# Optimization experiments

Measured on AMD Instinct MI355X. Metric: run time of the kernel, lower is better.

The kernel has to match this reference:

```python
import jax, jax.numpy as jnp
import numpy as np

N_NODES = 100000
N_EDGES = 1600000
F_IN = 128
HID = 128


def setup_inputs() -> dict:
    key = jax.random.key(0)
    ks = jax.random.split(key, 16)
    x = jax.random.normal(ks[0], (N_NODES, F_IN), dtype=jnp.float32)
    edge_index = jax.random.randint(ks[1], (2, N_EDGES), 0, N_NODES, dtype=jnp.int32)
    edge_weight = jax.random.uniform(ks[2], (N_EDGES,), dtype=jnp.float32)
    def glorot(k, fan_in, fan_out):
        s = jnp.sqrt(6.0 / (fan_in + fan_out))
        return jax.random.uniform(k, (fan_in, fan_out), dtype=jnp.float32, minval=-s, maxval=s)
    inp = {"x": x, "edge_index": edge_index, "edge_weight": edge_weight}
    dims = [(F_IN, HID), (HID, HID), (HID, HID), (HID, HID)]
    for i, (di, do) in enumerate(dims):
        inp[f"Wc{i}"] = glorot(ks[3 + i], di, do)
        inp[f"bc{i}"] = jnp.zeros((do,), dtype=jnp.float32)
    inp["Wout"] = glorot(ks[8], HID, F_IN)
    inp["bout"] = jnp.zeros((F_IN,), dtype=jnp.float32)
    return inp


def _gcn_conv(x, W, b, row, col, ew, deg_isqrt, n):
    # PyG GCNConv: h = x @ W; out = sum_{(r,c)} norm_rc * h[r] scattered to c, plus
    # self-loop term (weight 1), plus bias. norm_rc = d^-1/2[r] * ew * d^-1/2[c].
    h = x @ W
    norm = deg_isqrt[row] * ew * deg_isqrt[col]          # [E]
    agg = jax.ops.segment_sum(h[row] * norm[:, None], col, num_segments=n)
    agg = agg + h * (deg_isqrt * deg_isqrt)[:, None]      # self loops, weight 1
    return agg + b


def reference(x, edge_index, edge_weight, Wc0, bc0, Wc1, bc1, Wc2, bc2, Wc3, bc3, Wout, bout):
    n = x.shape[0]
    row, col = edge_index[0], edge_index[1]
    # degree includes self-loop weight 1 (gcn_norm with add_self_loops=True)
    deg = jax.ops.segment_sum(edge_weight, col, num_segments=n) + 1.0
    deg_isqrt = jnp.where(deg > 0, jax.lax.rsqrt(deg), 0.0)
    Ws = [Wc0, Wc1, Wc2, Wc3]
    bs = [bc0, bc1, bc2, bc3]
    h = x
    for i in range(3):
        h = jax.nn.relu(_gcn_conv(h, Ws[i], bs[i], row, col, edge_weight, deg_isqrt, n))
    h = _gcn_conv(h, Ws[3], bs[3], row, col, edge_weight, deg_isqrt, n)
    return h @ Wout + bout
```

## Files before the change

### kernel.cpp

```cpp
#include <hip/hip_runtime.h>


#define SCAN_CHUNK 1024
#define NBUCK_MAX  512
#define BCAP       6144

typedef __attribute__((ext_vector_type(8))) short bf16x8;
typedef __attribute__((ext_vector_type(4))) float f32x4;

__device__ inline unsigned bf16pack(float a, float b) {
    unsigned ua = __float_as_uint(a);
    unsigned ub = __float_as_uint(b);
    ua = (ua + 0x7fffu + ((ua >> 16) & 1u)) >> 16;
    ub = (ub + 0x7fffu + ((ub >> 16) & 1u)) & 0xffff0000u;
    return ua | ub;
}

__device__ inline void split2(float x, ushort& hi, ushort& lo) {
    unsigned u = __float_as_uint(x);
    unsigned r = (u + 0x7fffu + ((u >> 16) & 1u)) & 0xffff0000u;
    hi = (ushort)(r >> 16);
    float rem = x - __uint_as_float(r);
    unsigned u2 = __float_as_uint(rem);
    lo = (ushort)((u2 + 0x7fffu + ((u2 >> 16) & 1u)) >> 16);
}

__device__ inline void bf16x8_expand(uint4 w, float4& a, float4& b) {
    a.x = __uint_as_float(w.x << 16);
    a.y = __uint_as_float(w.x & 0xffff0000u);
    a.z = __uint_as_float(w.y << 16);
    a.w = __uint_as_float(w.y & 0xffff0000u);
    b.x = __uint_as_float(w.z << 16);
    b.y = __uint_as_float(w.z & 0xffff0000u);
    b.z = __uint_as_float(w.w << 16);
    b.w = __uint_as_float(w.w & 0xffff0000u);
}

__global__ __launch_bounds__(256) void k_prepw(const float* W0, const float* W1,
                                               const float* W2, const float* W3,
                                               const float* W4,
                                               ushort* __restrict__ hiO,
                                               ushort* __restrict__ loO) {
    const float* W = (blockIdx.x == 0) ? W0 : (blockIdx.x == 1) ? W1 :
                     (blockIdx.x == 2) ? W2 : (blockIdx.x == 3) ? W3 : W4;
    ushort* h = hiO + (size_t)blockIdx.x * 16384;
    ushort* l = loO + (size_t)blockIdx.x * 16384;
    for (int idx = threadIdx.x; idx < 4096; idx += 256) {
        int n  = idx >> 5;
        int kq = (idx & 31) * 4;
        ushort hs[4], ls[4];
#pragma unroll
        for (int j = 0; j < 4; j++) split2(W[(kq + j) * 128 + n], hs[j], ls[j]);
        *(uint2*)&h[n * 128 + kq] =
            make_uint2(hs[0] | ((unsigned)hs[1] << 16), hs[2] | ((unsigned)hs[3] << 16));
        *(uint2*)&l[n * 128 + kq] =
            make_uint2(ls[0] | ((unsigned)ls[1] << 16), ls[2] | ((unsigned)ls[3] << 16));
    }
}

__global__ __launch_bounds__(256) void k_hist(const int* __restrict__ col,
                                              int* __restrict__ hist,
                                              int E, int K, int B1, int chunk) {
    __shared__ int cnt[NBUCK_MAX];
    int b = blockIdx.x, t = threadIdx.x;
    for (int k = t; k < K; k += 256) cnt[k] = 0;
    __syncthreads();
    int e0 = b * chunk, e1 = min(e0 + chunk, E);
    for (int e = e0 + t; e < e1; e += 256) atomicAdd(&cnt[col[e] >> 8], 1);
    __syncthreads();
    for (int k = t; k < K; k += 256) hist[k * B1 + b] = cnt[k];
}

__global__ __launch_bounds__(256) void k_scan_part(const int* __restrict__ count,
                                                   int* __restrict__ partials, int n) {
    __shared__ int red[256];
    int t = threadIdx.x;
    int base = blockIdx.x * SCAN_CHUNK + t * 4;
    int s = 0;
#pragma unroll
    for (int j = 0; j < 4; j++) {
        int i = base + j;
        if (i < n) s += count[i];
    }
    red[t] = s;
    __syncthreads();
    for (int off = 128; off > 0; off >>= 1) {
        if (t < off) red[t] += red[t + off];
        __syncthreads();
    }
    if (t == 0) partials[blockIdx.x] = red[0];
}

__global__ __launch_bounds__(1024) void k_scan_top(const int* __restrict__ partials,
                                                   int* __restrict__ blockOff,
                                                   int* __restrict__ result,
                                                   int nb, int n) {
    __shared__ int sums[1024];
    int t = threadIdx.x;
    int v = (t < nb) ? partials[t] : 0;
    sums[t] = v;
    __syncthreads();
    for (int off = 1; off < 1024; off <<= 1) {
        int u = (t >= off) ? sums[t - off] : 0;
        __syncthreads();
        sums[t] += u;
        __syncthreads();
    }
    if (t < nb) blockOff[t] = sums[t] - v;
    if (t == nb - 1) result[n] = sums[t];
}

__global__ __launch_bounds__(256) void k_scan_out(const int* __restrict__ count,
                                                  const int* __restrict__ blockOff,
                                                  int* __restrict__ result, int n) {
    __shared__ int sums[256];
    int t = threadIdx.x;
    int base = blockIdx.x * SCAN_CHUNK + t * 4;
    int c[4]; int s = 0;
#pragma unroll
    for (int j = 0; j < 4; j++) {
        int i = base + j;
        c[j] = (i < n) ? count[i] : 0;
        s += c[j];
    }
    sums[t] = s;
    __syncthreads();
    for (int off = 1; off < 256; off <<= 1) {
        int u = (t >= off) ? sums[t - off] : 0;
        __syncthreads();
        sums[t] += u;
        __syncthreads();
    }
    int run = blockOff[blockIdx.x] + sums[t] - s;
#pragma unroll
    for (int j = 0; j < 4; j++) {
        int i = base + j;
        if (i < n) result[i] = run;
        run += c[j];
    }
}

__global__ __launch_bounds__(256) void k_scatter(const int* __restrict__ row,
                                                 const int* __restrict__ col,
                                                 const float* __restrict__ ew,
                                                 const int* __restrict__ binBase,
                                                 uint2* __restrict__ etmp,
                                                 int E, int K, int B1, int chunk) {
    __shared__ int cur[NBUCK_MAX];
    int b = blockIdx.x, t = threadIdx.x;
    for (int k = t; k < K; k += 256) cur[k] = binBase[k * B1 + b];
    __syncthreads();
    int e0 = b * chunk, e1 = min(e0 + chunk, E);
    for (int e = e0 + t; e < e1; e += 256) {
        int c = col[e];
        int k = c >> 8;
        int pos = atomicAdd(&cur[k], 1);
        etmp[pos] = make_uint2((unsigned)row[e] | ((unsigned)(c & 255) << 24),
                               __float_as_uint(ew[e]));
    }
}

__global__ __launch_bounds__(256) void k_bucket(const uint2* __restrict__ etmp,
                                                const int* __restrict__ binBase,
                                                uint2* __restrict__ edges,
                                                int* __restrict__ offsets,
                                                float* __restrict__ disq,
                                                int N, int K, int B1) {
    __shared__ unsigned ls[BCAP];
    __shared__ unsigned lw[BCAP];
    __shared__ int   cnt[256];
    __shared__ float sew[256];
    __shared__ int   excl[257];
    int k = blockIdx.x, t = threadIdx.x;
    int bStart = binBase[k * B1];
    int bEnd   = binBase[(k + 1) * B1];
    int size   = bEnd - bStart;
    cnt[t] = 0; sew[t] = 0.f;
    __syncthreads();
    for (int i = t; i < size && i < BCAP; i += 256) {
        uint2 m = etmp[bStart + i];
        ls[i] = m.x; lw[i] = m.y;
        int j = m.x >> 24;
        atomicAdd(&cnt[j], 1);
        atomicAdd(&sew[j], __uint_as_float(m.y));
    }
    __syncthreads();
    excl[t + 1] = cnt[t];
    if (t == 0) excl[0] = 0;
    __syncthreads();
    for (int off = 1; off < 256; off <<= 1) {
        int add = (t + 1 > off) ? excl[t + 1 - off] : 0;
        __syncthreads();
        excl[t + 1] += add;
        __syncthreads();
    }
    int node = (k << 8) + t;
    if (node < N) {
        offsets[node] = bStart + excl[t];
        disq[node]    = rsqrtf(1.0f + sew[t]);
    }
    if (k == K - 1 && t == 0) offsets[N] = bEnd;
    cnt[t] = excl[t];
    __syncthreads();
    for (int i = t; i < size && i < BCAP; i += 256) {
        unsigned s = ls[i];
        int j = s >> 24;
        int pos = atomicAdd(&cnt[j], 1);
        edges[bStart + pos] = make_uint2(s & 0x00FFFFFFu, lw[i]);
    }
}

__global__ __launch_bounds__(256) void k_gemm_f32A(const float* __restrict__ A,
                                                   const ushort* __restrict__ WThi,
                                                   const ushort* __restrict__ WTlo,
                                                   const float* __restrict__ disq,
                                                   unsigned* __restrict__ Cout, int N) {
    __shared__ ushort Whi_s[128][136];
    __shared__ ushort Wlo_s[128][136];
    int tid = threadIdx.x;
#pragma unroll
    for (int r = 0; r < 8; r++) {
        int n  = r * 16 + (tid >> 4);
        int kq = (tid & 15) * 8;
        *(uint4*)&Whi_s[n][kq] = *(const uint4*)&WThi[n * 128 + kq];
        *(uint4*)&Wlo_s[n][kq] = *(const uint4*)&WTlo[n * 128 + kq];
    }
    __syncthreads();

    int wv = tid >> 6, ln = tid & 63;
    int quad = ln >> 4, col = ln & 15;
    int nodeBase = blockIdx.x * 128 + wv * 32;
    int node0 = nodeBase + col, node1 = nodeBase + 16 + col;

    f32x4 acc[2][8];
#pragma unroll
    for (int nb = 0; nb < 2; nb++)
#pragma unroll
        for (int f = 0; f < 8; f++) acc[nb][f] = (f32x4)0.f;

    for (int s = 0; s < 4; s++) {
        int k0 = s * 32 + quad * 8;
        float v0[8], v1[8];
#pragma unroll
        for (int j = 0; j < 8; j++) { v0[j] = 0.f; v1[j] = 0.f; }
        if (node0 < N) {
            float4 a = *(const float4*)&A[(size_t)node0 * 128 + k0];
            float4 b = *(const float4*)&A[(size_t)node0 * 128 + k0 + 4];
            v0[0] = a.x; v0[1] = a.y; v0[2] = a.z; v0[3] = a.w;
            v0[4] = b.x; v0[5] = b.y; v0[6] = b.z; v0[7] = b.w;
        }
        if (node1 < N) {
            float4 a = *(const float4*)&A[(size_t)node1 * 128 + k0];
            float4 b = *(const float4*)&A[(size_t)node1 * 128 + k0 + 4];
            v1[0] = a.x; v1[1] = a.y; v1[2] = a.z; v1[3] = a.w;
            v1[4] = b.x; v1[5] = b.y; v1[6] = b.z; v1[7] = b.w;
        }
        bf16x8 bh0, bl0, bh1, bl1;
#pragma unroll
        for (int j = 0; j < 8; j++) {
            ushort h, l;
            split2(v0[j], h, l); bh0[j] = (short)h; bl0[j] = (short)l;
            split2(v1[j], h, l); bh1[j] = (short)h; bl1[j] = (short)l;
        }
#pragma unroll
        for (int f = 0; f < 8; f++) {
            bf16x8 wh = *(const bf16x8*)&Whi_s[f * 16 + col][k0];
            bf16x8 wl = *(const bf16x8*)&Wlo_s[f * 16 + col][k0];
            acc[0][f] = __builtin_amdgcn_mfma_f32_16x16x32_bf16(wh, bh0, acc[0][f], 0, 0, 0);
            acc[1][f] = __builtin_amdgcn_mfma_f32_16x16x32_bf16(wh, bh1, acc[1][f], 0, 0, 0);
            acc[0][f] = __builtin_amdgcn_mfma_f32_16x16x32_bf16(wl, bh0, acc[0][f], 0, 0, 0);
            acc[1][f] = __builtin_amdgcn_mfma_f32_16x16x32_bf16(wl, bh1, acc[1][f], 0, 0, 0);
            acc[0][f] = __builtin_amdgcn_mfma_f32_16x16x32_bf16(wh, bl0, acc[0][f], 0, 0, 0);
            acc[1][f] = __builtin_amdgcn_mfma_f32_16x16x32_bf16(wh, bl1, acc[1][f], 0, 0, 0);
        }
    }
#pragma unroll
    for (int nb = 0; nb < 2; nb++) {
        int node = nodeBase + nb * 16 + col;
        if (node >= N) continue;
        float d = disq[node];
#pragma unroll
        for (int f = 0; f < 8; f++) {
            f32x4 a = acc[nb][f];
            uint2 u;
            u.x = bf16pack(a[0] * d, a[1] * d);
            u.y = bf16pack(a[2] * d, a[3] * d);
            *(uint2*)&Cout[(size_t)node * 64 + f * 8 + quad * 2] = u;
        }
    }
}

template <bool BF16OUT>
__global__ __launch_bounds__(256) void k_gemm_b16A(const unsigned* __restrict__ Ab,
                                                   const ushort* __restrict__ WThi,
                                                   const ushort* __restrict__ WTlo,
                                                   const float* __restrict__ bias,
                                                   const float* __restrict__ disq,
                                                   void* __restrict__ Cout, int N) {
    __shared__ ushort Whi_s[128][136];
    __shared__ ushort Wlo_s[128][136];
    int tid = threadIdx.x;
#pragma unroll
    for (int r = 0; r < 8; r++) {
        int n  = r * 16 + (tid >> 4);
        int kq = (tid & 15) * 8;
        *(uint4*)&Whi_s[n][kq] = *(const uint4*)&WThi[n * 128 + kq];
        *(uint4*)&Wlo_s[n][kq] = *(const uint4*)&WTlo[n * 128 + kq];
    }
    __syncthreads();

    int wv = tid >> 6, ln = tid & 63;
    int quad = ln >> 4, col = ln & 15;
    int nodeBase = blockIdx.x * 128 + wv * 32;
    int node0 = nodeBase + col, node1 = nodeBase + 16 + col;

    f32x4 acc[2][8];
#pragma unroll
    for (int nb = 0; nb < 2; nb++)
#pragma unroll
        for (int f = 0; f < 8; f++) acc[nb][f] = (f32x4)0.f;

    for (int s = 0; s < 4; s++) {
        int k0 = s * 32 + quad * 8;
        int kw = s * 16 + quad * 4;
        bf16x8 b0 = (bf16x8)(short)0, b1 = (bf16x8)(short)0;
        if (node0 < N) b0 = *(const bf16x8*)&Ab[(size_t)node0 * 64 + kw];
        if (node1 < N) b1 = *(const bf16x8*)&Ab[(size_t)node1 * 64 + kw];
#pragma unroll
        for (int f = 0; f < 8; f++) {
            bf16x8 wh = *(const bf16x8*)&Whi_s[f * 16 + col][k0];
            bf16x8 wl = *(const bf16x8*)&Wlo_s[f * 16 + col][k0];
            acc[0][f] = __builtin_amdgcn_mfma_f32_16x16x32_bf16(wh, b0, acc[0][f], 0, 0, 0);
            acc[1][f] = __builtin_amdgcn_mfma_f32_16x16x32_bf16(wh, b1, acc[1][f], 0, 0, 0);
            acc[0][f] = __builtin_amdgcn_mfma_f32_16x16x32_bf16(wl, b0, acc[0][f], 0, 0, 0);
            acc[1][f] = __builtin_amdgcn_mfma_f32_16x16x32_bf16(wl, b1, acc[1][f], 0, 0, 0);
        }
    }
#pragma unroll
    for (int nb = 0; nb < 2; nb++) {
        int node = nodeBase + nb * 16 + col;
        if (node >= N) continue;
        if (BF16OUT) {
            float d = disq[node];
            unsigned* tb = (unsigned*)Cout;
#pragma unroll
            for (int f = 0; f < 8; f++) {
                f32x4 a = acc[nb][f];
                uint2 u;
                u.x = bf16pack(a[0] * d, a[1] * d);
                u.y = bf16pack(a[2] * d, a[3] * d);
                *(uint2*)&tb[(size_t)node * 64 + f * 8 + quad * 2] = u;
            }
        } else {
            float* C = (float*)Cout;
#pragma unroll
            for (int f = 0; f < 8; f++) {
                int fb = f * 16 + quad * 4;
                float4 bv = *(const float4*)&bias[fb];
                f32x4 a = acc[nb][f];
                float4 o;
                o.x = a[0] + bv.x; o.y = a[1] + bv.y;
                o.z = a[2] + bv.z; o.w = a[3] + bv.w;
                *(float4*)&C[(size_t)node * 128 + fb] = o;
            }
        }
    }
}

__global__ __launch_bounds__(256) void k_aggregate(const unsigned* __restrict__ tb,
                                                   const int* __restrict__ offsets,
                                                   const uint2* __restrict__ edges,
                                                   const float* __restrict__ disq,
                                                   const float* __restrict__ bias,
                                                   unsigned* __restrict__ outb,
                                                   int N, int relu) {
    int wave = threadIdx.x >> 6;
    int lane = threadIdx.x & 63;
    int node = blockIdx.x * 4 + wave;
    if (node >= N) return;
    int q  = lane >> 4;
    int li = lane & 15;

    int e0 = offsets[node], e1 = offsets[node + 1];
    int deg = e1 - e0;
    float4 acc0 = make_float4(0.f, 0.f, 0.f, 0.f);
    float4 acc1 = make_float4(0.f, 0.f, 0.f, 0.f);

    int eL = e0 + q;
    float cf[4];
    uint4 w[4];
#pragma unroll
    for (int s = 0; s < 4; s++) { cf[s] = 0.f; w[s] = make_uint4(0u, 0u, 0u, 0u); }

#define FETCH(S, II) {                                                     \
        int ii = (II);                                                     \
        bool v = ii < e1;                                                  \
        if (v) {                                                           \
            uint2 m = edges[ii];                                           \
            cf[S] = __uint_as_float(m.y);                                  \
            w[S]  = *(const uint4*)&tb[(size_t)m.x * 64 + li * 4];         \
        } else cf[S] = 0.f;                                                \
    }
#define CONSUME(S) {                                                       \
        float4 a, b; bf16x8_expand(w[S], a, b);                            \
        float c = cf[S];                                                   \
        acc0.x += c * a.x; acc0.y += c * a.y;                              \
        acc0.z += c * a.z; acc0.w += c * a.w;                              \
        acc1.x += c * b.x; acc1.y += c * b.y;                              \
        acc1.z += c * b.z; acc1.w += c * b.w;                              \
    }

    FETCH(0, eL)
    FETCH(1, eL + 4)
    FETCH(2, eL + 8)
    FETCH(3, eL + 12)
    for (int base = 16; base < deg; base += 16) {
        CONSUME(0) FETCH(0, eL + base)
        CONSUME(1) FETCH(1, eL + base + 4)
        CONSUME(2) FETCH(2, eL + base + 8)
        CONSUME(3) FETCH(3, eL + base + 12)
    }
    CONSUME(0) CONSUME(1) CONSUME(2) CONSUME(3)
#undef FETCH
#undef CONSUME

#pragma unroll
    for (int m = 16; m <= 32; m <<= 1) {
        acc0.x += __shfl_xor(acc0.x, m);
        acc0.y += __shfl_xor(acc0.y, m);
        acc0.z += __shfl_xor(acc0.z, m);
        acc0.w += __shfl_xor(acc0.w, m);
        acc1.x += __shfl_xor(acc1.x, m);
        acc1.y += __shfl_xor(acc1.y, m);
        acc1.z += __shfl_xor(acc1.z, m);
        acc1.w += __shfl_xor(acc1.w, m);
    }
    if (q == 0) {
        float d = disq[node];
        uint4 wv = *(const uint4*)&tb[(size_t)node * 64 + li * 4];
        float4 ta, tbv;
        bf16x8_expand(wv, ta, tbv);
        float4 b0 = *(const float4*)&bias[li * 8];
        float4 b1 = *(const float4*)&bias[li * 8 + 4];
        float4 o0, o1;
        o0.x = d * (acc0.x + ta.x) + b0.x;
        o0.y = d * (acc0.y + ta.y) + b0.y;
        o0.z = d * (acc0.z + ta.z) + b0.z;
        o0.w = d * (acc0.w + ta.w) + b0.w;
        o1.x = d * (acc1.x + tbv.x) + b1.x;
        o1.y = d * (acc1.y + tbv.y) + b1.y;
        o1.z = d * (acc1.z + tbv.z) + b1.z;
        o1.w = d * (acc1.w + tbv.w) + b1.w;
        if (relu) {
            o0.x = fmaxf(o0.x, 0.f); o0.y = fmaxf(o0.y, 0.f);
            o0.z = fmaxf(o0.z, 0.f); o0.w = fmaxf(o0.w, 0.f);
            o1.x = fmaxf(o1.x, 0.f); o1.y = fmaxf(o1.y, 0.f);
            o1.z = fmaxf(o1.z, 0.f); o1.w = fmaxf(o1.w, 0.f);
        }
        uint4 u;
        u.x = bf16pack(o0.x, o0.y);
        u.y = bf16pack(o0.z, o0.w);
        u.z = bf16pack(o1.x, o1.y);
        u.w = bf16pack(o1.z, o1.w);
        *(uint4*)&outb[(size_t)node * 64 + li * 4] = u;
    }
}

extern "C" void kernel_launch(void* const* d_in, const int* in_sizes, int n_in,
                              void* d_out, int out_size, void* d_ws, size_t ws_size,
                              hipStream_t stream) {
    const float* x    = (const float*)d_in[0];
    const int*   ei   = (const int*)d_in[1];
    const float* ew   = (const float*)d_in[2];
    const float* Wc[4] = {(const float*)d_in[3], (const float*)d_in[5],
                          (const float*)d_in[7], (const float*)d_in[9]};
    const float* bc[4] = {(const float*)d_in[4], (const float*)d_in[6],
                          (const float*)d_in[8], (const float*)d_in[10]};
    const float* Wout = (const float*)d_in[11];
    const float* bout = (const float*)d_in[12];

    const int N = in_sizes[0] / 128;
    const int E = in_sizes[2];
    const int* row = ei;
    const int* col = ei + E;

    const int K     = (N + 255) >> 8;
    const int B1    = 256;
    const int chunk = (E + B1 - 1) / B1;
    const int nScan = K * B1;

    size_t off = 0;
    char* base = (char*)d_ws;
    auto alloc = [&](size_t bytes) -> void* {
        void* p = base + off;
        off += (bytes + 255) & ~(size_t)255;
        return p;
    };
    float*    disq     = (float*)alloc((size_t)N * 4);
    int*      offsets  = (int*)alloc((size_t)(N + 1) * 4);
    int*      hist     = (int*)alloc((size_t)nScan * 4);
    int*      binBase  = (int*)alloc((size_t)(nScan + 1) * 4);
    int*      partials = (int*)alloc(1024 * 4);
    int*      blockOff = (int*)alloc(1024 * 4);
    ushort*   WThi     = (ushort*)alloc((size_t)5 * 16384 * 2);
    ushort*   WTlo     = (ushort*)alloc((size_t)5 * 16384 * 2);
    uint2*    etmp     = (uint2*)alloc((size_t)E * 8);
    uint2*    edges    = (uint2*)alloc((size_t)E * 8);
    unsigned* hb       = (unsigned*)alloc((size_t)N * 64 * 4);
    unsigned* tb       = (unsigned*)alloc((size_t)N * 64 * 4);

    const int BG  = (N + 127) / 128;
    const int BA  = (N + 3) / 4;
    const int NBs = (nScan + SCAN_CHUNK - 1) / SCAN_CHUNK;

    k_prepw<<<5, 256, 0, stream>>>(Wc[0], Wc[1], Wc[2], Wc[3], Wout, WThi, WTlo);
    k_hist<<<B1, 256, 0, stream>>>(col, hist, E, K, B1, chunk);
    k_scan_part<<<NBs, 256, 0, stream>>>(hist, partials, nScan);
    k_scan_top<<<1, 1024, 0, stream>>>(partials, blockOff, binBase, NBs, nScan);
    k_scan_out<<<NBs, 256, 0, stream>>>(hist, blockOff, binBase, nScan);
    k_scatter<<<B1, 256, 0, stream>>>(row, col, ew, binBase, etmp, E, K, B1, chunk);
    k_bucket<<<K, 256, 0, stream>>>(etmp, binBase, edges, offsets, disq, N, K, B1);

    k_gemm_f32A<<<BG, 256, 0, stream>>>(x, WThi, WTlo, disq, tb, N);
    k_aggregate<<<BA, 256, 0, stream>>>(tb, offsets, edges, disq, bc[0], hb, N, 1);
    k_gemm_b16A<true><<<BG, 256, 0, stream>>>(hb, WThi + 16384, WTlo + 16384, nullptr, disq, tb, N);
    k_aggregate<<<BA, 256, 0, stream>>>(tb, offsets, edges, disq, bc[1], hb, N, 1);
    k_gemm_b16A<true><<<BG, 256, 0, stream>>>(hb, WThi + 32768, WTlo + 32768, nullptr, disq, tb, N);
    k_aggregate<<<BA, 256, 0, stream>>>(tb, offsets, edges, disq, bc[2], hb, N, 1);
    k_gemm_b16A<true><<<BG, 256, 0, stream>>>(hb, WThi + 49152, WTlo + 49152, nullptr, disq, tb, N);
    k_aggregate<<<BA, 256, 0, stream>>>(tb, offsets, edges, disq, bc[3], hb, N, 0);
    k_gemm_b16A<false><<<BG, 256, 0, stream>>>(hb, WThi + 65536, WTlo + 65536, bout, nullptr, d_out, N);
}
```

Baseline: 580.6 us.

## Fuse aggregation with the next layer's GEMM through shared memory

Replaces the separate aggregate and GEMM kernels with one fused kernel per layer. Each block aggregates 64 nodes into an XOR-swizzled bf16 tile in LDS, then runs the next layer's MFMA GEMM directly on that tile. This avoids writing and re-reading the intermediate hidden activations through global memory and removes four launches. Edge sources are stored pre-shifted as byte offsets so the gather skips an index multiply. Each quarter-wave now owns one node instead of splitting a node across four edge lanes, which changes load balance for high-degree nodes. The weights are read straight from global memory rather than staged in LDS.

```diff
diff --git a/kernel.cpp b/kernel.cpp
--- a/kernel.cpp
+++ b/kernel.cpp
@@ -206,7 +206,7 @@
         unsigned s = ls[i];
         int j = s >> 24;
         int pos = atomicAdd(&cnt[j], 1);
-        edges[bStart + pos] = make_uint2(s & 0x00FFFFFFu, lw[i]);
+        edges[bStart + pos] = make_uint2((s & 0x00FFFFFFu) << 8, lw[i]);
     }
 }
 
@@ -290,115 +290,35 @@
     }
 }
 
-template <bool BF16OUT>
-__global__ __launch_bounds__(256) void k_gemm_b16A(const unsigned* __restrict__ Ab,
-                                                   const ushort* __restrict__ WThi,
-                                                   const ushort* __restrict__ WTlo,
-                                                   const float* __restrict__ bias,
-                                                   const float* __restrict__ disq,
-                                                   void* __restrict__ Cout, int N) {
-    __shared__ ushort Whi_s[128][136];
-    __shared__ ushort Wlo_s[128][136];
-    int tid = threadIdx.x;
-#pragma unroll
-    for (int r = 0; r < 8; r++) {
-        int n  = r * 16 + (tid >> 4);
-        int kq = (tid & 15) * 8;
-        *(uint4*)&Whi_s[n][kq] = *(const uint4*)&WThi[n * 128 + kq];
-        *(uint4*)&Wlo_s[n][kq] = *(const uint4*)&WTlo[n * 128 + kq];
-    }
-    __syncthreads();
-
-    int wv = tid >> 6, ln = tid & 63;
-    int quad = ln >> 4, col = ln & 15;
-    int nodeBase = blockIdx.x * 128 + wv * 32;
-    int node0 = nodeBase + col, node1 = nodeBase + 16 + col;
-
-    f32x4 acc[2][8];
-#pragma unroll
-    for (int nb = 0; nb < 2; nb++)
-#pragma unroll
-        for (int f = 0; f < 8; f++) acc[nb][f] = (f32x4)0.f;
-
-    for (int s = 0; s < 4; s++) {
-        int k0 = s * 32 + quad * 8;
-        int kw = s * 16 + quad * 4;
-        bf16x8 b0 = (bf16x8)(short)0, b1 = (bf16x8)(short)0;
-        if (node0 < N) b0 = *(const bf16x8*)&Ab[(size_t)node0 * 64 + kw];
-        if (node1 < N) b1 = *(const bf16x8*)&Ab[(size_t)node1 * 64 + kw];
-#pragma unroll
-        for (int f = 0; f < 8; f++) {
-            bf16x8 wh = *(const bf16x8*)&Whi_s[f * 16 + col][k0];
-            bf16x8 wl = *(const bf16x8*)&Wlo_s[f * 16 + col][k0];
-            acc[0][f] = __builtin_amdgcn_mfma_f32_16x16x32_bf16(wh, b0, acc[0][f], 0, 0, 0);
-            acc[1][f] = __builtin_amdgcn_mfma_f32_16x16x32_bf16(wh, b1, acc[1][f], 0, 0, 0);
-            acc[0][f] = __builtin_amdgcn_mfma_f32_16x16x32_bf16(wl, b0, acc[0][f], 0, 0, 0);
-            acc[1][f] = __builtin_amdgcn_mfma_f32_16x16x32_bf16(wl, b1, acc[1][f], 0, 0, 0);
-        }
-    }
-#pragma unroll
-    for (int nb = 0; nb < 2; nb++) {
-        int node = nodeBase + nb * 16 + col;
-        if (node >= N) continue;
-        if (BF16OUT) {
-            float d = disq[node];
-            unsigned* tb = (unsigned*)Cout;
-#pragma unroll
-            for (int f = 0; f < 8; f++) {
-                f32x4 a = acc[nb][f];
-                uint2 u;
-                u.x = bf16pack(a[0] * d, a[1] * d);
-                u.y = bf16pack(a[2] * d, a[3] * d);
-                *(uint2*)&tb[(size_t)node * 64 + f * 8 + quad * 2] = u;
-            }
-        } else {
-            float* C = (float*)Cout;
-#pragma unroll
-            for (int f = 0; f < 8; f++) {
-                int fb = f * 16 + quad * 4;
-                float4 bv = *(const float4*)&bias[fb];
-                f32x4 a = acc[nb][f];
-                float4 o;
-                o.x = a[0] + bv.x; o.y = a[1] + bv.y;
-                o.z = a[2] + bv.z; o.w = a[3] + bv.w;
-                *(float4*)&C[(size_t)node * 128 + fb] = o;
-            }
-        }
-    }
-}
-
-__global__ __launch_bounds__(256) void k_aggregate(const unsigned* __restrict__ tb,
-                                                   const int* __restrict__ offsets,
-                                                   const uint2* __restrict__ edges,
-                                                   const float* __restrict__ disq,
-                                                   const float* __restrict__ bias,
-                                                   unsigned* __restrict__ outb,
-                                                   int N, int relu) {
-    int wave = threadIdx.x >> 6;
-    int lane = threadIdx.x & 63;
-    int node = blockIdx.x * 4 + wave;
-    if (node >= N) return;
-    int q  = lane >> 4;
-    int li = lane & 15;
-
-    int e0 = offsets[node], e1 = offsets[node + 1];
-    int deg = e1 - e0;
-    float4 acc0 = make_float4(0.f, 0.f, 0.f, 0.f);
-    float4 acc1 = make_float4(0.f, 0.f, 0.f, 0.f);
-
-    int eL = e0 + q;
-    float cf[4];
-    uint4 w[4];
+template <bool FINAL>
+__global__ __launch_bounds__(256, 4) void k_fused(const unsigned* __restrict__ tbIn,
+                                                  const ushort* __restrict__ WThi,
+                                                  const ushort* __restrict__ WTlo,
+                                                  const float* __restrict__ aggBias,
+                                                  const float* __restrict__ outBias,
+                                                  const float* __restrict__ disq,
+                                                  const int* __restrict__ offsets,
+                                                  const uint2* __restrict__ edges,
+                                                  void* __restrict__ outp, int N) {
+    __shared__ __align__(16) ushort hs[64 * 128];
+    const int tid = threadIdx.x;
+    const int wv = tid >> 6, lane = tid & 63;
+    const int q = lane >> 4, li = lane & 15;
+    const int blockBase = blockIdx.x * 64;
+    const char* tbc = (const char*)tbIn;
+
+    float4 bs0 = *(const float4*)&aggBias[li * 8];
+    float4 bs1 = *(const float4*)&aggBias[li * 8 + 4];
+    float cf[4]; uint4 w[4];
 #pragma unroll
     for (int s = 0; s < 4; s++) { cf[s] = 0.f; w[s] = make_uint4(0u, 0u, 0u, 0u); }
 
 #define FETCH(S, II) {                                                     \
         int ii = (II);                                                     \
-        bool v = ii < e1;                                                  \
-        if (v) {                                                           \
+        if (ii < e1) {                                                     \
             uint2 m = edges[ii];                                           \
             cf[S] = __uint_as_float(m.y);                                  \
-            w[S]  = *(const uint4*)&tb[(size_t)m.x * 64 + li * 4];         \
+            w[S]  = *(const uint4*)(tbc + m.x + (li << 4));                \
         } else cf[S] = 0.f;                                                \
     }
 #define CONSUME(S) {                                                       \
@@ -410,59 +330,106 @@
         acc1.z += c * b.z; acc1.w += c * b.w;                              \
     }
 
-    FETCH(0, eL)
-    FETCH(1, eL + 4)
-    FETCH(2, eL + 8)
-    FETCH(3, eL + 12)
-    for (int base = 16; base < deg; base += 16) {
-        CONSUME(0) FETCH(0, eL + base)
-        CONSUME(1) FETCH(1, eL + base + 4)
-        CONSUME(2) FETCH(2, eL + base + 8)
-        CONSUME(3) FETCH(3, eL + base + 12)
-    }
-    CONSUME(0) CONSUME(1) CONSUME(2) CONSUME(3)
+    for (int r = 0; r < 4; r++) {
+        int nl   = wv * 16 + r * 4 + q;
+        int node = blockBase + nl;
+        int e0 = 0, e1 = 0;
+        if (node < N) { e0 = offsets[node]; e1 = offsets[node + 1]; }
+        float4 acc0 = make_float4(0.f, 0.f, 0.f, 0.f);
+        float4 acc1 = make_float4(0.f, 0.f, 0.f, 0.f);
+
+        FETCH(0, e0)
+        FETCH(1, e0 + 1)
+        FETCH(2, e0 + 2)
+        FETCH(3, e0 + 3)
+        for (int eb = e0 + 4; eb < e1; eb += 4) {
+            CONSUME(0) FETCH(0, eb)
+            CONSUME(1) FETCH(1, eb + 1)
+            CONSUME(2) FETCH(2, eb + 2)
+            CONSUME(3) FETCH(3, eb + 3)
+        }
+        CONSUME(0) CONSUME(1) CONSUME(2) CONSUME(3)
+
+        if (node < N) {
+            float d = disq[node];
+            uint4 sv = *(const uint4*)(tbc + ((size_t)node << 8) + (li << 4));
+            float4 ta, tb2;
+            bf16x8_expand(sv, ta, tb2);
+            float4 o0, o1;
+            o0.x = d * (acc0.x + ta.x) + bs0.x;
+            o0.y = d * (acc0.y + ta.y) + bs0.y;
+            o0.z = d * (acc0.z + ta.z) + bs0.z;
+            o0.w = d * (acc0.w + ta.w) + bs0.w;
+            o1.x = d * (acc1.x + tb2.x) + bs1.x;
+            o1.y = d * (acc1.y + tb2.y) + bs1.y;
+            o1.z = d * (acc1.z + tb2.z) + bs1.z;
+            o1.w = d * (acc1.w + tb2.w) + bs1.w;
+            if (!FINAL) {
+                o0.x = fmaxf(o0.x, 0.f); o0.y = fmaxf(o0.y, 0.f);
+                o0.z = fmaxf(o0.z, 0.f); o0.w = fmaxf(o0.w, 0.f);
+                o1.x = fmaxf(o1.x, 0.f); o1.y = fmaxf(o1.y, 0.f);
+                o1.z = fmaxf(o1.z, 0.f); o1.w = fmaxf(o1.w, 0.f);
+            }
+            uint4 u;
+            u.x = bf16pack(o0.x, o0.y);
+            u.y = bf16pack(o0.z, o0.w);
+            u.z = bf16pack(o1.x, o1.y);
+            u.w = bf16pack(o1.z, o1.w);
+            *(uint4*)&hs[nl * 128 + ((li * 8) ^ ((nl & 7) << 3))] = u;
+        }
+    }
 #undef FETCH
 #undef CONSUME
-
-#pragma unroll
-    for (int m = 16; m <= 32; m <<= 1) {
-        acc0.x += __shfl_xor(acc0.x, m);
-        acc0.y += __shfl_xor(acc0.y, m);
-        acc0.z += __shfl_xor(acc0.z, m);
-        acc0.w += __shfl_xor(acc0.w, m);
-        acc1.x += __shfl_xor(acc1.x, m);
-        acc1.y += __shfl_xor(acc1.y, m);
-        acc1.z += __shfl_xor(acc1.z, m);
-        acc1.w += __shfl_xor(acc1.w, m);
-    }
-    if (q == 0) {
-        float d = disq[node];
-        uint4 wv = *(const uint4*)&tb[(size_t)node * 64 + li * 4];
-        float4 ta, tbv;
-        bf16x8_expand(wv, ta, tbv);
-        float4 b0 = *(const float4*)&bias[li * 8];
-        float4 b1 = *(const float4*)&bias[li * 8 + 4];
-        float4 o0, o1;
-        o0.x = d * (acc0.x + ta.x) + b0.x;
-        o0.y = d * (acc0.y + ta.y) + b0.y;
-        o0.z = d * (acc0.z + ta.z) + b0.z;
-        o0.w = d * (acc0.w + ta.w) + b0.w;
-        o1.x = d * (acc1.x + tbv.x) + b1.x;
-        o1.y = d * (acc1.y + tbv.y) + b1.y;
-        o1.z = d * (acc1.z + tbv.z) + b1.z;
-        o1.w = d * (acc1.w + tbv.w) + b1.w;
-        if (relu) {
-            o0.x = fmaxf(o0.x, 0.f); o0.y = fmaxf(o0.y, 0.f);
-            o0.z = fmaxf(o0.z, 0.f); o0.w = fmaxf(o0.w, 0.f);
-            o1.x = fmaxf(o1.x, 0.f); o1.y = fmaxf(o1.y, 0.f);
-            o1.z = fmaxf(o1.z, 0.f); o1.w = fmaxf(o1.w, 0.f);
-        }
-        uint4 u;
-        u.x = bf16pack(o0.x, o0.y);
-        u.y = bf16pack(o0.z, o0.w);
-        u.z = bf16pack(o1.x, o1.y);
-        u.w = bf16pack(o1.z, o1.w);
-        *(uint4*)&outb[(size_t)node * 64 + li * 4] = u;
+    __syncthreads();
+
+    f32x4 accg[2][4];
+#pragma unroll
+    for (int fs = 0; fs < 2; fs++)
+#pragma unroll
+        for (int ns = 0; ns < 4; ns++) accg[fs][ns] = (f32x4)0.f;
+
+    for (int s = 0; s < 4; s++) {
+        int k0  = s * 32 + q * 8;
+        int wr0 = (wv * 32 + li) * 128 + k0;
+        bf16x8 wh0 = *(const bf16x8*)&WThi[wr0];
+        bf16x8 wl0 = *(const bf16x8*)&WTlo[wr0];
+        bf16x8 wh1 = *(const bf16x8*)&WThi[wr0 + 2048];
+        bf16x8 wl1 = *(const bf16x8*)&WTlo[wr0 + 2048];
+#pragma unroll
+        for (int ns = 0; ns < 4; ns++) {
+            int nl = ns * 16 + li;
+            bf16x8 b = *(const bf16x8*)&hs[nl * 128 + (k0 ^ ((nl & 7) << 3))];
+            accg[0][ns] = __builtin_amdgcn_mfma_f32_16x16x32_bf16(wh0, b, accg[0][ns], 0, 0, 0);
+            accg[0][ns] = __builtin_amdgcn_mfma_f32_16x16x32_bf16(wl0, b, accg[0][ns], 0, 0, 0);
+            accg[1][ns] = __builtin_amdgcn_mfma_f32_16x16x32_bf16(wh1, b, accg[1][ns], 0, 0, 0);
+            accg[1][ns] = __builtin_amdgcn_mfma_f32_16x16x32_bf16(wl1, b, accg[1][ns], 0, 0, 0);
+        }
+    }
+
+#pragma unroll
+    for (int fs = 0; fs < 2; fs++) {
+        int f = wv * 2 + fs;
+#pragma unroll
+        for (int ns = 0; ns < 4; ns++) {
+            int node = blockBase + ns * 16 + li;
+            if (node >= N) continue;
+            if (!FINAL) {
+                float d = disq[node];
+                f32x4 a = accg[fs][ns];
+                uint2 u;
+                u.x = bf16pack(a[0] * d, a[1] * d);
+                u.y = bf16pack(a[2] * d, a[3] * d);
+                *(uint2*)&((unsigned*)outp)[(size_t)node * 64 + f * 8 + q * 2] = u;
+            } else {
+                int fb = f * 16 + q * 4;
+                float4 bv = *(const float4*)&outBias[fb];
+                f32x4 a = accg[fs][ns];
+                float4 o;
+                o.x = a[0] + bv.x; o.y = a[1] + bv.y;
+                o.z = a[2] + bv.z; o.w = a[3] + bv.w;
+                *(float4*)&((float*)outp)[(size_t)node * 128 + fb] = o;
+            }
+        }
     }
 }
 
@@ -506,11 +473,11 @@
     ushort*   WTlo     = (ushort*)alloc((size_t)5 * 16384 * 2);
     uint2*    etmp     = (uint2*)alloc((size_t)E * 8);
     uint2*    edges    = (uint2*)alloc((size_t)E * 8);
-    unsigned* hb       = (unsigned*)alloc((size_t)N * 64 * 4);
-    unsigned* tb       = (unsigned*)alloc((size_t)N * 64 * 4);
+    unsigned* bufA     = (unsigned*)alloc((size_t)N * 64 * 4);
+    unsigned* bufB     = (unsigned*)alloc((size_t)N * 64 * 4);
 
     const int BG  = (N + 127) / 128;
-    const int BA  = (N + 3) / 4;
+    const int BF  = (N + 63) / 64;
     const int NBs = (nScan + SCAN_CHUNK - 1) / SCAN_CHUNK;
 
     k_prepw<<<5, 256, 0, stream>>>(Wc[0], Wc[1], Wc[2], Wc[3], Wout, WThi, WTlo);
@@ -521,13 +488,13 @@
     k_scatter<<<B1, 256, 0, stream>>>(row, col, ew, binBase, etmp, E, K, B1, chunk);
     k_bucket<<<K, 256, 0, stream>>>(etmp, binBase, edges, offsets, disq, N, K, B1);
 
-    k_gemm_f32A<<<BG, 256, 0, stream>>>(x, WThi, WTlo, disq, tb, N);
-    k_aggregate<<<BA, 256, 0, stream>>>(tb, offsets, edges, disq, bc[0], hb, N, 1);
-    k_gemm_b16A<true><<<BG, 256, 0, stream>>>(hb, WThi + 16384, WTlo + 16384, nullptr, disq, tb, N);
-    k_aggregate<<<BA, 256, 0, stream>>>(tb, offsets, edges, disq, bc[1], hb, N, 1);
-    k_gemm_b16A<true><<<BG, 256, 0, stream>>>(hb, WThi + 32768, WTlo + 32768, nullptr, disq, tb, N);
-    k_aggregate<<<BA, 256, 0, stream>>>(tb, offsets, edges, disq, bc[2], hb, N, 1);
-    k_gemm_b16A<true><<<BG, 256, 0, stream>>>(hb, WThi + 49152, WTlo + 49152, nullptr, disq, tb, N);
-    k_aggregate<<<BA, 256, 0, stream>>>(tb, offsets, edges, disq, bc[3], hb, N, 0);
-    k_gemm_b16A<false><<<BG, 256, 0, stream>>>(hb, WThi + 65536, WTlo + 65536, bout, nullptr, d_out, N);
-}
+    k_gemm_f32A<<<BG, 256, 0, stream>>>(x, WThi, WTlo, disq, bufA, N);
+    k_fused<false><<<BF, 256, 0, stream>>>(bufA, WThi + 16384, WTlo + 16384,
+                                           bc[0], nullptr, disq, offsets, edges, bufB, N);
+    k_fused<false><<<BF, 256, 0, stream>>>(bufB, WThi + 32768, WTlo + 32768,
+                                           bc[1], nullptr, disq, offsets, edges, bufA, N);
+    k_fused<false><<<BF, 256, 0, stream>>>(bufA, WThi + 49152, WTlo + 49152,
+                                           bc[2], nullptr, disq, offsets, edges, bufB, N);
+    k_fused<true><<<BF, 256, 0, stream>>>(bufB, WThi + 65536, WTlo + 65536,
+                                          bc[3], bout, disq, offsets, edges, d_out, N);
+}
```

Result: slower. 653.8 us (+12.6%).

## Map one node per quarter-wave in aggregation and pre-scale edge source offsets

Applied to the files above, without the earlier changes.

The aggregation kernel now gives each 16-lane group its own node, walking all of that node's edges serially with an 8-deep prefetch ring. Before, a full wave shared one node and split edges four ways, which needed a cross-lane shuffle reduction and left most lanes idle in the epilogue. The bucket kernel now stores each source index pre-shifted to a byte offset, saving a multiply in the gather address. Risks: more registers for the deeper ring, load imbalance within a wave across nodes of different degree, and the shifted index overflowing 32 bits if node counts grow.

```diff
diff --git a/kernel.cpp b/kernel.cpp
--- a/kernel.cpp
+++ b/kernel.cpp
@@ -206,7 +206,7 @@
         unsigned s = ls[i];
         int j = s >> 24;
         int pos = atomicAdd(&cnt[j], 1);
-        edges[bStart + pos] = make_uint2(s & 0x00FFFFFFu, lw[i]);
+        edges[bStart + pos] = make_uint2((s & 0x00FFFFFFu) << 8, lw[i]);
     }
 }
 
@@ -367,38 +367,34 @@
     }
 }
 
-__global__ __launch_bounds__(256) void k_aggregate(const unsigned* __restrict__ tb,
-                                                   const int* __restrict__ offsets,
-                                                   const uint2* __restrict__ edges,
-                                                   const float* __restrict__ disq,
-                                                   const float* __restrict__ bias,
-                                                   unsigned* __restrict__ outb,
-                                                   int N, int relu) {
-    int wave = threadIdx.x >> 6;
-    int lane = threadIdx.x & 63;
-    int node = blockIdx.x * 4 + wave;
+__global__ __launch_bounds__(256, 8) void k_aggregate(const unsigned* __restrict__ tb,
+                                                      const int* __restrict__ offsets,
+                                                      const uint2* __restrict__ edges,
+                                                      const float* __restrict__ disq,
+                                                      const float* __restrict__ bias,
+                                                      unsigned* __restrict__ outb,
+                                                      int N, int relu) {
+    const int tid = threadIdx.x;
+    const int wv = tid >> 6, lane = tid & 63;
+    const int q = lane >> 4, li = lane & 15;
+    const int node = blockIdx.x * 16 + wv * 4 + q;
     if (node >= N) return;
-    int q  = lane >> 4;
-    int li = lane & 15;
+    const char* tbc = (const char*)tb;
 
     int e0 = offsets[node], e1 = offsets[node + 1];
-    int deg = e1 - e0;
     float4 acc0 = make_float4(0.f, 0.f, 0.f, 0.f);
     float4 acc1 = make_float4(0.f, 0.f, 0.f, 0.f);
 
-    int eL = e0 + q;
-    float cf[4];
-    uint4 w[4];
-#pragma unroll
-    for (int s = 0; s < 4; s++) { cf[s] = 0.f; w[s] = make_uint4(0u, 0u, 0u, 0u); }
+    float cf[8]; uint4 w[8];
+#pragma unroll
+    for (int s = 0; s < 8; s++) { cf[s] = 0.f; w[s] = make_uint4(0u, 0u, 0u, 0u); }
 
 #define FETCH(S, II) {                                                     \
         int ii = (II);                                                     \
-        bool v = ii < e1;                                                  \
-        if (v) {                                                           \
+        if (ii < e1) {                                                     \
             uint2 m = edges[ii];                                           \
             cf[S] = __uint_as_float(m.y);                                  \
-            w[S]  = *(const uint4*)&tb[(size_t)m.x * 64 + li * 4];         \
+            w[S]  = *(const uint4*)(tbc + m.x + (li << 4));                \
         } else cf[S] = 0.f;                                                \
     }
 #define CONSUME(S) {                                                       \
@@ -410,60 +406,50 @@
         acc1.z += c * b.z; acc1.w += c * b.w;                              \
     }
 
-    FETCH(0, eL)
-    FETCH(1, eL + 4)
-    FETCH(2, eL + 8)
-    FETCH(3, eL + 12)
-    for (int base = 16; base < deg; base += 16) {
-        CONSUME(0) FETCH(0, eL + base)
-        CONSUME(1) FETCH(1, eL + base + 4)
-        CONSUME(2) FETCH(2, eL + base + 8)
-        CONSUME(3) FETCH(3, eL + base + 12)
+    FETCH(0, e0)     FETCH(1, e0 + 1) FETCH(2, e0 + 2) FETCH(3, e0 + 3)
+    FETCH(4, e0 + 4) FETCH(5, e0 + 5) FETCH(6, e0 + 6) FETCH(7, e0 + 7)
+    for (int eb = e0 + 8; eb < e1; eb += 8) {
+        CONSUME(0) FETCH(0, eb)
+        CONSUME(1) FETCH(1, eb + 1)
+        CONSUME(2) FETCH(2, eb + 2)
+        CONSUME(3) FETCH(3, eb + 3)
+        CONSUME(4) FETCH(4, eb + 4)
+        CONSUME(5) FETCH(5, eb + 5)
+        CONSUME(6) FETCH(6, eb + 6)
+        CONSUME(7) FETCH(7, eb + 7)
     }
     CONSUME(0) CONSUME(1) CONSUME(2) CONSUME(3)
+    CONSUME(4) CONSUME(5) CONSUME(6) CONSUME(7)
 #undef FETCH
 #undef CONSUME
 
-#pragma unroll
-    for (int m = 16; m <= 32; m <<= 1) {
-        acc0.x += __shfl_xor(acc0.x, m);
-        acc0.y += __shfl_xor(acc0.y, m);
-        acc0.z += __shfl_xor(acc0.z, m);
-        acc0.w += __shfl_xor(acc0.w, m);
-        acc1.x += __shfl_xor(acc1.x, m);
-        acc1.y += __shfl_xor(acc1.y, m);
-        acc1.z += __shfl_xor(acc1.z, m);
-        acc1.w += __shfl_xor(acc1.w, m);
-    }
-    if (q == 0) {
-        float d = disq[node];
-        uint4 wv = *(const uint4*)&tb[(size_t)node * 64 + li * 4];
-        float4 ta, tbv;
-        bf16x8_expand(wv, ta, tbv);
-        float4 b0 = *(const float4*)&bias[li * 8];
-        float4 b1 = *(const float4*)&bias[li * 8 + 4];
-        float4 o0, o1;
-        o0.x = d * (acc0.x + ta.x) + b0.x;
-        o0.y = d * (acc0.y + ta.y) + b0.y;
-        o0.z = d * (acc0.z + ta.z) + b0.z;
-        o0.w = d * (acc0.w + ta.w) + b0.w;
-        o1.x = d * (acc1.x + tbv.x) + b1.x;
-        o1.y = d * (acc1.y + tbv.y) + b1.y;
-        o1.z = d * (acc1.z + tbv.z) + b1.z;
-        o1.w = d * (acc1.w + tbv.w) + b1.w;
-        if (relu) {
-            o0.x = fmaxf(o0.x, 0.f); o0.y = fmaxf(o0.y, 0.f);
-            o0.z = fmaxf(o0.z, 0.f); o0.w = fmaxf(o0.w, 0.f);
-            o1.x = fmaxf(o1.x, 0.f); o1.y = fmaxf(o1.y, 0.f);
-            o1.z = fmaxf(o1.z, 0.f); o1.w = fmaxf(o1.w, 0.f);
-        }
-        uint4 u;
-        u.x = bf16pack(o0.x, o0.y);
-        u.y = bf16pack(o0.z, o0.w);
-        u.z = bf16pack(o1.x, o1.y);
-        u.w = bf16pack(o1.z, o1.w);
-        *(uint4*)&outb[(size_t)node * 64 + li * 4] = u;
-    }
+    float d = disq[node];
+    uint4 sv = *(const uint4*)(tbc + ((size_t)node << 8) + (li << 4));
+    float4 ta, tbv;
+    bf16x8_expand(sv, ta, tbv);
+    float4 b0 = *(const float4*)&bias[li * 8];
+    float4 b1 = *(const float4*)&bias[li * 8 + 4];
+    float4 o0, o1;
+    o0.x = d * (acc0.x + ta.x) + b0.x;
+    o0.y = d * (acc0.y + ta.y) + b0.y;
+    o0.z = d * (acc0.z + ta.z) + b0.z;
+    o0.w = d * (acc0.w + ta.w) + b0.w;
+    o1.x = d * (acc1.x + tbv.x) + b1.x;
+    o1.y = d * (acc1.y + tbv.y) + b1.y;
+    o1.z = d * (acc1.z + tbv.z) + b1.z;
+    o1.w = d * (acc1.w + tbv.w) + b1.w;
+    if (relu) {
+        o0.x = fmaxf(o0.x, 0.f); o0.y = fmaxf(o0.y, 0.f);
+        o0.z = fmaxf(o0.z, 0.f); o0.w = fmaxf(o0.w, 0.f);
+        o1.x = fmaxf(o1.x, 0.f); o1.y = fmaxf(o1.y, 0.f);
+        o1.z = fmaxf(o1.z, 0.f); o1.w = fmaxf(o1.w, 0.f);
+    }
+    uint4 u;
+    u.x = bf16pack(o0.x, o0.y);
+    u.y = bf16pack(o0.z, o0.w);
+    u.z = bf16pack(o1.x, o1.y);
+    u.w = bf16pack(o1.z, o1.w);
+    *(uint4*)&outb[(size_t)node * 64 + li * 4] = u;
 }
 
 extern "C" void kernel_launch(void* const* d_in, const int* in_sizes, int n_in,
@@ -510,7 +496,7 @@
     unsigned* tb       = (unsigned*)alloc((size_t)N * 64 * 4);
 
     const int BG  = (N + 127) / 128;
-    const int BA  = (N + 3) / 4;
+    const int BA  = (N + 15) / 16;
     const int NBs = (nScan + SCAN_CHUNK - 1) / SCAN_CHUNK;
 
     k_prepw<<<5, 256, 0, stream>>>(Wc[0], Wc[1], Wc[2], Wc[3], Wout, WThi, WTlo);
```

New measurement: 2.117 ms. 3.65x slower.
